# Performance work log

Hardware: AMD Instinct MI355X
Metric: run time of the kernel (lower is better)

The kernel has to match this reference:

```python
import jax, jax.numpy as jnp
import numpy as np

B, T, D, H = 2, 2048, 1024, 16
HD = D // H  # head dim = 64


def setup_inputs() -> dict:
    key = jax.random.key(0)
    ks = jax.random.split(key, 8)
    scale = 0.02
    return {
        "query_states": jax.random.normal(ks[0], (B, T, D), jnp.float32),
        "key_states": jax.random.normal(ks[1], (B, T, D), jnp.float32),
        "query_mask": jnp.ones((B, T), jnp.float32),
        "key_mask": jnp.ones((B, T), jnp.float32),
        "Wq": jax.random.normal(ks[2], (D, D), jnp.float32) * scale,
        "bq": jnp.zeros((D,), jnp.float32),
        "Wk": jax.random.normal(ks[3], (D, D), jnp.float32) * scale,
        "bk": jnp.zeros((D,), jnp.float32),
        "Wv": jax.random.normal(ks[4], (D, D), jnp.float32) * scale,
        "bv": jnp.zeros((D,), jnp.float32),
        "mask_future": 1,
    }


def _split_heads(x):  # [B,T,D] -> [B,H,T,HD]
    return x.reshape(B, T, H, HD).transpose(0, 2, 1, 3)


def reference(query_states, key_states, query_mask, key_mask, Wq, bq, Wk, bk, Wv, bv, mask_future):
    q = _split_heads(query_states @ Wq.T + bq)
    k = _split_heads(key_states @ Wk.T + bk)
    v = _split_heads(key_states @ Wv.T + bv)
    # [B,H,T,T]
    scores = jnp.einsum("bhqd,bhkd->bhqk", q, k) / jnp.sqrt(jnp.float32(HD))
    scores = scores + (1.0 - key_mask)[:, None, None, :] * -10000.0
    if mask_future:
        causal = (1.0 - jnp.tril(jnp.ones((T, T), jnp.float32))) * -10000.0
        scores = scores + causal[None, None, :, :]
    probs = jax.nn.softmax(scores, axis=-1)
    probs = probs * query_mask[:, None, :, None]  # post-softmax query mask
    ctx = jnp.einsum("bhqk,bhkd->bhqd", probs, v)
    return ctx.transpose(0, 2, 1, 3).reshape(B, T, D)
```

## Files before the change

kernel.cpp:

```cpp
#include <hip/hip_runtime.h>
#include <hip/hip_bf16.h>
#include <stdint.h>

typedef __attribute__((ext_vector_type(8))) short short8;
typedef __attribute__((ext_vector_type(4))) short short4_t;
typedef __attribute__((ext_vector_type(4))) float f32x4;

#define B_ 2
#define T_ 2048
#define D_ 1024
#define H_ 16
#define HD_ 64
#define BT_ 4096
#define NKT64 32

__device__ __forceinline__ unsigned short f2bf(float f) {
    union { float f; uint32_t u; } v; v.f = f;
    uint32_t u = v.u;
    uint32_t r = (u + 0x7fffu + ((u >> 16) & 1u)) >> 16;
    return (unsigned short)r;
}

__device__ __forceinline__ uint32_t pack2(float a, float b) {
    return (uint32_t)f2bf(a) | ((uint32_t)f2bf(b) << 16);
}

__device__ __forceinline__ void gld16(const void* g, void* l) {
    __builtin_amdgcn_global_load_lds((const __attribute__((address_space(1))) void*)g,
                                     (__attribute__((address_space(3))) void*)l, 16, 0, 0);
}

__device__ __forceinline__ int swz(int x) { return x ^ (((x >> 7) & 7) << 4); }

__global__ __launch_bounds__(256) void cvt2(const float* __restrict__ s0, unsigned short* __restrict__ d0,
                                            const float* __restrict__ s1, unsigned short* __restrict__ d1,
                                            const float* __restrict__ kmask, float* __restrict__ kpen_g,
                                            int n8) {
    int i = blockIdx.x * 256 + threadIdx.x;
    if (blockIdx.y == 2) {
        if (i < B_ * T_) kpen_g[i] = (1.0f - kmask[i]) * -10000.0f;
        return;
    }
    const float* src = blockIdx.y ? s1 : s0;
    unsigned short* dst = blockIdx.y ? d1 : d0;
    if (i >= n8) return;
    const float4* s = (const float4*)src + (size_t)i * 2;
    float4 a = s[0], b4 = s[1];
    short8 o;
    o[0] = (short)f2bf(a.x);  o[1] = (short)f2bf(a.y);
    o[2] = (short)f2bf(a.z);  o[3] = (short)f2bf(a.w);
    o[4] = (short)f2bf(b4.x); o[5] = (short)f2bf(b4.y);
    o[6] = (short)f2bf(b4.z); o[7] = (short)f2bf(b4.w);
    *(short8*)(dst + (size_t)i * 8) = o;
}

__global__ __launch_bounds__(256) void cvt3(const float* __restrict__ s0, unsigned short* __restrict__ d0,
                                            const float* __restrict__ s1, unsigned short* __restrict__ d1,
                                            const float* __restrict__ s2, unsigned short* __restrict__ d2,
                                            int n8) {
    const float* src = blockIdx.y == 0 ? s0 : (blockIdx.y == 1 ? s1 : s2);
    unsigned short* dst = blockIdx.y == 0 ? d0 : (blockIdx.y == 1 ? d1 : d2);
    int i = blockIdx.x * 256 + threadIdx.x;
    if (i >= n8) return;
    const float4* s = (const float4*)src + (size_t)i * 2;
    float4 a = s[0], b4 = s[1];
    short8 o;
    o[0] = (short)f2bf(a.x);  o[1] = (short)f2bf(a.y);
    o[2] = (short)f2bf(a.z);  o[3] = (short)f2bf(a.w);
    o[4] = (short)f2bf(b4.x); o[5] = (short)f2bf(b4.y);
    o[6] = (short)f2bf(b4.z); o[7] = (short)f2bf(b4.w);
    *(short8*)(dst + (size_t)i * 8) = o;
}

__global__ __launch_bounds__(256) void qkv_gemm_fused(const unsigned short* __restrict__ xq,
                                                      const unsigned short* __restrict__ xk,
                                                      const unsigned short* __restrict__ wq,
                                                      const unsigned short* __restrict__ wk,
                                                      const unsigned short* __restrict__ wv,
                                                      const float* __restrict__ bq,
                                                      const float* __restrict__ bk,
                                                      const float* __restrict__ bv,
                                                      unsigned short* __restrict__ q_ws,
                                                      unsigned short* __restrict__ k_ws,
                                                      unsigned short* __restrict__ v8_ws) {
    __shared__ unsigned short Al[128 * 32];
    __shared__ unsigned short Bl[128 * 32];
    const int K = D_;
    int z = blockIdx.z;
    const unsigned short* X = (z == 0) ? xq : xk;
    const unsigned short* W = (z == 0) ? wq : (z == 1 ? wk : wv);
    const float* bias = (z == 0) ? bq : (z == 1 ? bk : bv);

    int m0 = blockIdx.x * 128, n0 = blockIdx.y * 128;
    int tid = threadIdx.x, lane = tid & 63, w = tid >> 6;
    int wr = w >> 1, wc = w & 1;

    f32x4 acc[4][4];
#pragma unroll
    for (int i = 0; i < 4; i++)
#pragma unroll
        for (int j = 0; j < 4; j++) acc[i][j] = (f32x4){0.f, 0.f, 0.f, 0.f};

    int srow0 = (lane >> 2);
    int skch = (lane & 3) * 8;

    for (int kt = 0; kt < K / 32; ++kt) {
        int kb = kt * 32;
#pragma unroll
        for (int t = 0; t < 2; ++t) {
            int ins = w * 2 + t;
            int row = ins * 16 + srow0;
            gld16(X + (size_t)(m0 + row) * K + kb + skch, (char*)Al + ins * 1024);
            gld16(W + (size_t)(n0 + row) * K + kb + skch, (char*)Bl + ins * 1024);
        }
        __syncthreads();
        short8 af[4], bf[4];
#pragma unroll
        for (int mi = 0; mi < 4; mi++)
            af[mi] = *(const short8*)(Al + (wr * 64 + mi * 16 + (lane & 15)) * 32 + (lane >> 4) * 8);
#pragma unroll
        for (int ni = 0; ni < 4; ni++)
            bf[ni] = *(const short8*)(Bl + (wc * 64 + ni * 16 + (lane & 15)) * 32 + (lane >> 4) * 8);
#pragma unroll
        for (int mi = 0; mi < 4; mi++)
#pragma unroll
            for (int ni = 0; ni < 4; ni++)
                acc[mi][ni] = __builtin_amdgcn_mfma_f32_16x16x32_bf16(af[mi], bf[ni], acc[mi][ni], 0, 0, 0);
        __syncthreads();
    }

    if (z < 2) {
        unsigned short* outp = (z == 0) ? q_ws : k_ws;
#pragma unroll
        for (int ni = 0; ni < 4; ni++) {
            int n = n0 + wc * 64 + ni * 16 + (lane & 15);
            float bv2 = bias[n];
            int h = n >> 6, hd = n & 63;
#pragma unroll
            for (int mi = 0; mi < 4; mi++) {
#pragma unroll
                for (int r = 0; r < 4; r++) {
                    int m = m0 + wr * 64 + mi * 16 + (lane >> 4) * 4 + r;
                    int b = m >> 11, t = m & (T_ - 1);
                    outp[((size_t)(b * H_ + h) * T_ + t) * HD_ + hd] = f2bf(acc[mi][ni][r] + bv2);
                }
            }
        }
    } else {
#pragma unroll
        for (int ni = 0; ni < 4; ni++) {
            int n = n0 + wc * 64 + ni * 16 + (lane & 15);
            float bv2 = bias[n];
            int h = n >> 6, hd = n & 63;
#pragma unroll
            for (int mi = 0; mi < 4; mi++) {
                int m = m0 + wr * 64 + mi * 16 + (lane >> 4) * 4;
                int b = m >> 11, t = m & (T_ - 1);
                short4_t pk;
#pragma unroll
                for (int r = 0; r < 4; r++) pk[r] = (short)f2bf(acc[mi][ni][r] + bv2);
                *(short4_t*)(v8_ws + (((size_t)(b * H_ + h) * 256 + (t >> 3)) * HD_ + hd) * 8 + (t & 7)) = pk;
            }
        }
    }
}

__global__ __launch_bounds__(256) void attn(const unsigned short* __restrict__ q_ws,
                                            const unsigned short* __restrict__ k_ws,
                                            const unsigned short* __restrict__ v8_ws,
                                            const float* __restrict__ qmask,
                                            const float* __restrict__ kpen_g,
                                            const int* __restrict__ mfp,
                                            float* __restrict__ out) {
    __shared__ char SH[4 * 2048 * 4 + 1024];

    int w = threadIdx.x >> 6;
    int lane = threadIdx.x & 63;
    int lg = lane >> 4, q = lane & 15;
    int bid = blockIdx.x;
    int qt = 63 - (bid >> 5);
    int bh = bid & 31;
    int b = bh >> 4, h = bh & 15;
    int q0 = qt * 32;
    int mf = mfp[0];
    int nkt = mf ? (qt >> 1) + 1 : NKT64;
    char* Pw = SH + w * 4096;

    int base = nkt >> 2, rem = nkt & 3;
    int cnt = base + (w < rem ? 1 : 0);
    int start = w * base + (w < rem ? w : rem);

    short8 qf[2][2];
#pragma unroll
    for (int m = 0; m < 2; m++) {
        const unsigned short* qp = q_ws + ((size_t)bh * T_ + q0 + m * 16 + q) * HD_ + lg * 8;
        qf[m][0] = *(const short8*)qp;
        qf[m][1] = *(const short8*)(qp + 32);
    }

    f32x4 o[2][4];
#pragma unroll
    for (int m = 0; m < 2; m++)
#pragma unroll
        for (int i = 0; i < 4; i++) o[m][i] = (f32x4){0.f, 0.f, 0.f, 0.f};
    float mrow[2] = {-1e30f, -1e30f};
    float lrow[2] = {0.f, 0.f};

    const float* kpenb = kpen_g + b * T_;

    for (int kt = start; kt < start + cnt; ++kt) {
        int kv0 = kt * 64;

        f32x4 s[2][4];
        __builtin_amdgcn_s_setprio(1);
#pragma unroll
        for (int nb = 0; nb < 4; nb++) {
            const unsigned short* kp = k_ws + ((size_t)bh * T_ + kv0 + nb * 16 + q) * HD_ + lg * 8;
            short8 kf0 = *(const short8*)kp;
            short8 kf1 = *(const short8*)(kp + 32);
#pragma unroll
            for (int m = 0; m < 2; m++) {
                f32x4 z = (f32x4){0.f, 0.f, 0.f, 0.f};
                z = __builtin_amdgcn_mfma_f32_16x16x32_bf16(kf0, qf[m][0], z, 0, 0, 0);
                z = __builtin_amdgcn_mfma_f32_16x16x32_bf16(kf1, qf[m][1], z, 0, 0, 0);
                s[m][nb] = z;
            }
        }
        __builtin_amdgcn_s_setprio(0);

        short8 vf[4][2];
        const unsigned short* vbase = v8_ws + (((size_t)bh * 256 + (kv0 >> 3) + lg) * 64 + q) * 8;
#pragma unroll
        for (int nbh = 0; nbh < 4; nbh++) {
            vf[nbh][0] = *(const short8*)(vbase + nbh * 128);
            vf[nbh][1] = *(const short8*)(vbase + nbh * 128 + 2048);
        }

        f32x4 kp4[4];
#pragma unroll
        for (int nb = 0; nb < 4; nb++)
            kp4[nb] = *(const f32x4*)(kpenb + kv0 + nb * 16 + lg * 4);

        bool diag = mf && (kv0 + 63 > q0);
        float sc[2];
#pragma unroll
        for (int m = 0; m < 2; m++) {
            int qg = q0 + m * 16 + q;
#pragma unroll
            for (int nb = 0; nb < 4; nb++) {
#pragma unroll
                for (int r = 0; r < 4; r++) {
                    float v = s[m][nb][r] * 0.125f + kp4[nb][r];
                    if (diag) {
                        int kvg = kv0 + nb * 16 + lg * 4 + r;
                        v = (kvg > qg) ? v - 10000.0f : v;
                    }
                    s[m][nb][r] = v;
                }
            }
            float xm = fmaxf(
                fmaxf(fmaxf(fmaxf(s[m][0][0], s[m][0][1]), fmaxf(s[m][0][2], s[m][0][3])),
                      fmaxf(fmaxf(s[m][1][0], s[m][1][1]), fmaxf(s[m][1][2], s[m][1][3]))),
                fmaxf(fmaxf(fmaxf(s[m][2][0], s[m][2][1]), fmaxf(s[m][2][2], s[m][2][3])),
                      fmaxf(fmaxf(s[m][3][0], s[m][3][1]), fmaxf(s[m][3][2], s[m][3][3]))));
            xm = fmaxf(xm, __shfl_xor(xm, 16));
            xm = fmaxf(xm, __shfl_xor(xm, 32));
            float mn = fmaxf(mrow[m], xm);
            sc[m] = __expf(mrow[m] - mn);
            mrow[m] = mn;

#pragma unroll
            for (int nb = 0; nb < 4; nb++)
#pragma unroll
                for (int r = 0; r < 4; r++) s[m][nb][r] = __expf(s[m][nb][r] - mn);

            float rs = ((s[m][0][0] + s[m][0][1]) + (s[m][0][2] + s[m][0][3]))
                     + ((s[m][1][0] + s[m][1][1]) + (s[m][1][2] + s[m][1][3]))
                     + ((s[m][2][0] + s[m][2][1]) + (s[m][2][2] + s[m][2][3]))
                     + ((s[m][3][0] + s[m][3][1]) + (s[m][3][2] + s[m][3][3]));
            rs += __shfl_xor(rs, 16);
            rs += __shfl_xor(rs, 32);
            lrow[m] = lrow[m] * sc[m] + rs;

#pragma unroll
            for (int nbh = 0; nbh < 4; nbh++)
#pragma unroll
                for (int r = 0; r < 4; r++) o[m][nbh][r] *= sc[m];

#pragma unroll
            for (int nb = 0; nb < 4; nb++) {
                uint2 ww;
                ww.x = pack2(s[m][nb][0], s[m][nb][1]);
                ww.y = pack2(s[m][nb][2], s[m][nb][3]);
                *(uint2*)(Pw + m * 2048 + swz(q * 128 + nb * 32 + lg * 8)) = ww;
            }
        }

        short8 pf[2][2];
#pragma unroll
        for (int m = 0; m < 2; m++) {
            pf[m][0] = *(const short8*)(Pw + m * 2048 + swz(q * 128 + lg * 16));
            pf[m][1] = *(const short8*)(Pw + m * 2048 + swz(q * 128 + 64 + lg * 16));
        }

        __builtin_amdgcn_s_setprio(1);
#pragma unroll
        for (int nbh = 0; nbh < 4; nbh++) {
#pragma unroll
            for (int m = 0; m < 2; m++) {
                o[m][nbh] = __builtin_amdgcn_mfma_f32_16x16x32_bf16(vf[nbh][0], pf[m][0], o[m][nbh], 0, 0, 0);
                o[m][nbh] = __builtin_amdgcn_mfma_f32_16x16x32_bf16(vf[nbh][1], pf[m][1], o[m][nbh], 0, 0, 0);
            }
        }
        __builtin_amdgcn_s_setprio(0);
    }

    __syncthreads();
    float* OS = (float*)SH;
    float* ML = (float*)(SH + 32768);
#pragma unroll
    for (int m = 0; m < 2; m++)
#pragma unroll
        for (int nbh = 0; nbh < 4; nbh++)
            *(f32x4*)(OS + w * 2048 + ((m * 4 + nbh) * 64 + lane) * 4) = o[m][nbh];
    if (lane < 16) {
#pragma unroll
        for (int m = 0; m < 2; m++) {
            float2 ml2 = make_float2(mrow[m], lrow[m]);
            *(float2*)(ML + ((w * 2 + m) * 16 + q) * 2) = ml2;
        }
    }
    __syncthreads();

#pragma unroll
    for (int m = 0; m < 2; m++) {
        float2 ml0 = *(const float2*)(ML + ((0 * 2 + m) * 16 + q) * 2);
        float2 ml1 = *(const float2*)(ML + ((1 * 2 + m) * 16 + q) * 2);
        float2 ml2 = *(const float2*)(ML + ((2 * 2 + m) * 16 + q) * 2);
        float2 ml3 = *(const float2*)(ML + ((3 * 2 + m) * 16 + q) * 2);
        float M = fmaxf(fmaxf(ml0.x, ml1.x), fmaxf(ml2.x, ml3.x));
        float e0 = __expf(ml0.x - M), e1 = __expf(ml1.x - M);
        float e2 = __expf(ml2.x - M), e3 = __expf(ml3.x - M);
        float den = ml0.y * e0 + ml1.y * e1 + ml2.y * e2 + ml3.y * e3;

        f32x4 O0 = *(const f32x4*)(OS + 0 * 2048 + ((m * 4 + w) * 64 + lane) * 4);
        f32x4 O1 = *(const f32x4*)(OS + 1 * 2048 + ((m * 4 + w) * 64 + lane) * 4);
        f32x4 O2 = *(const f32x4*)(OS + 2 * 2048 + ((m * 4 + w) * 64 + lane) * 4);
        f32x4 O3 = *(const f32x4*)(OS + 3 * 2048 + ((m * 4 + w) * 64 + lane) * 4);

        int qg = q0 + m * 16 + q;
        float inv = qmask[b * T_ + qg] / den;
        f32x4 ov;
#pragma unroll
        for (int r = 0; r < 4; r++)
            ov[r] = (O0[r] * e0 + O1[r] * e1 + O2[r] * e2 + O3[r] * e3) * inv;
        *(f32x4*)(out + ((size_t)(b * T_ + qg)) * D_ + h * 64 + w * 16 + lg * 4) = ov;
    }
}

extern "C" void kernel_launch(void* const* d_in, const int* in_sizes, int n_in,
                              void* d_out, int out_size, void* d_ws, size_t ws_size,
                              hipStream_t stream) {
    const float* xq = (const float*)d_in[0];
    const float* xk = (const float*)d_in[1];
    const float* qmask = (const float*)d_in[2];
    const float* kmask = (const float*)d_in[3];
    const float* Wq = (const float*)d_in[4];
    const float* bq = (const float*)d_in[5];
    const float* Wk = (const float*)d_in[6];
    const float* bk = (const float*)d_in[7];
    const float* Wv = (const float*)d_in[8];
    const float* bv = (const float*)d_in[9];
    const int* mf = (const int*)d_in[10];
    float* out = (float*)d_out;

    char* ws = (char*)d_ws;
    unsigned short* xq_bf = (unsigned short*)(ws);
    unsigned short* xk_bf = (unsigned short*)(ws + (8u << 20));
    unsigned short* wq_bf = (unsigned short*)(ws + (16u << 20));
    unsigned short* wk_bf = (unsigned short*)(ws + (18u << 20));
    unsigned short* wv_bf = (unsigned short*)(ws + (20u << 20));
    unsigned short* q_ws  = (unsigned short*)(ws + (22u << 20));
    unsigned short* k_ws  = (unsigned short*)(ws + (30u << 20));
    unsigned short* v8_ws = (unsigned short*)(ws + (38u << 20));
    float* kpen_g         = (float*)(ws + (46u << 20));

    cvt2<<<dim3(BT_ * D_ / 8 / 256, 3), 256, 0, stream>>>(xq, xq_bf, xk, xk_bf, kmask, kpen_g, BT_ * D_ / 8);
    cvt3<<<dim3(D_ * D_ / 8 / 256, 3), 256, 0, stream>>>(Wq, wq_bf, Wk, wk_bf, Wv, wv_bf, D_ * D_ / 8);

    dim3 gg(BT_ / 128, D_ / 128, 3);
    qkv_gemm_fused<<<gg, 256, 0, stream>>>(xq_bf, xk_bf, wq_bf, wk_bf, wv_bf, bq, bk, bv,
                                           q_ws, k_ws, v8_ws);

    attn<<<2048, 256, 0, stream>>>(q_ws, k_ws, v8_ws, qmask, kpen_g, mf, out);
}
```

Before: 127.6 us.

## Fold softmax scale and log2e into Q, use exp2 and skip unchanged rescales

Pre-multiplies Q by scale*log2(e) in the projection epilogue and scales the mask penalties to match, so the attention loop can use raw exp2 without a per-score multiply. The online-softmax rescale of the running sum and output accumulators now runs only when some lane's row max increases. P is packed with the hardware bf16 pair conversion instead of manual rounding. These changes cut VALU work in the softmax inner loop, at the cost of a wave-level branch and slightly different rounding of Q.

```diff
diff --git a/kernel.cpp b/kernel.cpp
--- a/kernel.cpp
+++ b/kernel.cpp
@@ -14,6 +14,9 @@
 #define BT_ 4096
 #define NKT64 32
 
+#define QSCALE 0.1803368801111601f
+#define PEN2 14426.950408889634f
+
 __device__ __forceinline__ unsigned short f2bf(float f) {
     union { float f; uint32_t u; } v; v.f = f;
     uint32_t u = v.u;
@@ -21,8 +24,10 @@
     return (unsigned short)r;
 }
 
-__device__ __forceinline__ uint32_t pack2(float a, float b) {
-    return (uint32_t)f2bf(a) | ((uint32_t)f2bf(b) << 16);
+__device__ __forceinline__ uint32_t cvtpk(float a, float b) {
+    union { __hip_bfloat162 h; uint32_t u; } cv;
+    cv.h = __float22bfloat162_rn(make_float2(a, b));
+    return cv.u;
 }
 
 __device__ __forceinline__ void gld16(const void* g, void* l) {
@@ -38,7 +43,7 @@
                                             int n8) {
     int i = blockIdx.x * 256 + threadIdx.x;
     if (blockIdx.y == 2) {
-        if (i < B_ * T_) kpen_g[i] = (1.0f - kmask[i]) * -10000.0f;
+        if (i < B_ * T_) kpen_g[i] = (1.0f - kmask[i]) * -PEN2;
         return;
     }
     const float* src = blockIdx.y ? s1 : s0;
@@ -131,6 +136,7 @@
 
     if (z < 2) {
         unsigned short* outp = (z == 0) ? q_ws : k_ws;
+        float osc = (z == 0) ? QSCALE : 1.0f;
 #pragma unroll
         for (int ni = 0; ni < 4; ni++) {
             int n = n0 + wc * 64 + ni * 16 + (lane & 15);
@@ -142,7 +148,7 @@
                 for (int r = 0; r < 4; r++) {
                     int m = m0 + wr * 64 + mi * 16 + (lane >> 4) * 4 + r;
                     int b = m >> 11, t = m & (T_ - 1);
-                    outp[((size_t)(b * H_ + h) * T_ + t) * HD_ + hd] = f2bf(acc[mi][ni][r] + bv2);
+                    outp[((size_t)(b * H_ + h) * T_ + t) * HD_ + hd] = f2bf((acc[mi][ni][r] + bv2) * osc);
                 }
             }
         }
@@ -242,7 +248,6 @@
             kp4[nb] = *(const f32x4*)(kpenb + kv0 + nb * 16 + lg * 4);
 
         bool diag = mf && (kv0 + 63 > q0);
-        float sc[2];
 #pragma unroll
         for (int m = 0; m < 2; m++) {
             int qg = q0 + m * 16 + q;
@@ -250,10 +255,10 @@
             for (int nb = 0; nb < 4; nb++) {
 #pragma unroll
                 for (int r = 0; r < 4; r++) {
-                    float v = s[m][nb][r] * 0.125f + kp4[nb][r];
+                    float v = s[m][nb][r] + kp4[nb][r];
                     if (diag) {
                         int kvg = kv0 + nb * 16 + lg * 4 + r;
-                        v = (kvg > qg) ? v - 10000.0f : v;
+                        v = (kvg > qg) ? v - PEN2 : v;
                     }
                     s[m][nb][r] = v;
                 }
@@ -265,14 +270,23 @@
                       fmaxf(fmaxf(s[m][3][0], s[m][3][1]), fmaxf(s[m][3][2], s[m][3][3]))));
             xm = fmaxf(xm, __shfl_xor(xm, 16));
             xm = fmaxf(xm, __shfl_xor(xm, 32));
-            float mn = fmaxf(mrow[m], xm);
-            sc[m] = __expf(mrow[m] - mn);
-            mrow[m] = mn;
+
+            if (__any(xm > mrow[m])) {
+                float mn = fmaxf(mrow[m], xm);
+                float sc = __builtin_amdgcn_exp2f(mrow[m] - mn);
+                mrow[m] = mn;
+                lrow[m] *= sc;
+#pragma unroll
+                for (int nbh = 0; nbh < 4; nbh++)
+#pragma unroll
+                    for (int r = 0; r < 4; r++) o[m][nbh][r] *= sc;
+            }
 
 #pragma unroll
             for (int nb = 0; nb < 4; nb++)
 #pragma unroll
-                for (int r = 0; r < 4; r++) s[m][nb][r] = __expf(s[m][nb][r] - mn);
+                for (int r = 0; r < 4; r++)
+                    s[m][nb][r] = __builtin_amdgcn_exp2f(s[m][nb][r] - mrow[m]);
 
             float rs = ((s[m][0][0] + s[m][0][1]) + (s[m][0][2] + s[m][0][3]))
                      + ((s[m][1][0] + s[m][1][1]) + (s[m][1][2] + s[m][1][3]))
@@ -280,18 +294,13 @@
                      + ((s[m][3][0] + s[m][3][1]) + (s[m][3][2] + s[m][3][3]));
             rs += __shfl_xor(rs, 16);
             rs += __shfl_xor(rs, 32);
-            lrow[m] = lrow[m] * sc[m] + rs;
-
-#pragma unroll
-            for (int nbh = 0; nbh < 4; nbh++)
-#pragma unroll
-                for (int r = 0; r < 4; r++) o[m][nbh][r] *= sc[m];
+            lrow[m] += rs;
 
 #pragma unroll
             for (int nb = 0; nb < 4; nb++) {
                 uint2 ww;
-                ww.x = pack2(s[m][nb][0], s[m][nb][1]);
-                ww.y = pack2(s[m][nb][2], s[m][nb][3]);
+                ww.x = cvtpk(s[m][nb][0], s[m][nb][1]);
+                ww.y = cvtpk(s[m][nb][2], s[m][nb][3]);
                 *(uint2*)(Pw + m * 2048 + swz(q * 128 + nb * 32 + lg * 8)) = ww;
             }
         }
@@ -339,8 +348,8 @@
         float2 ml2 = *(const float2*)(ML + ((2 * 2 + m) * 16 + q) * 2);
         float2 ml3 = *(const float2*)(ML + ((3 * 2 + m) * 16 + q) * 2);
         float M = fmaxf(fmaxf(ml0.x, ml1.x), fmaxf(ml2.x, ml3.x));
-        float e0 = __expf(ml0.x - M), e1 = __expf(ml1.x - M);
-        float e2 = __expf(ml2.x - M), e3 = __expf(ml3.x - M);
+        float e0 = __builtin_amdgcn_exp2f(ml0.x - M), e1 = __builtin_amdgcn_exp2f(ml1.x - M);
+        float e2 = __builtin_amdgcn_exp2f(ml2.x - M), e3 = __builtin_amdgcn_exp2f(ml3.x - M);
         float den = ml0.y * e0 + ml1.y * e1 + ml2.y * e2 + ml3.y * e3;
 
         f32x4 O0 = *(const f32x4*)(OS + 0 * 2048 + ((m * 4 + w) * 64 + lane) * 4);
```

Measured after the change: 125.4 us. No clear change (-1.7%).
